# Kernel optimization log

Measured on AMD Instinct MI355X. Metric: run time of the kernel, lower is better.

## Reference

```python
import jax, jax.numpy as jnp
import numpy as np

N_AGENTS = 10000
N_TARGETS = 10000
N_EDGES = 320000
IN_CH = 8
DS = 32          # n_channels // 2 per GAT preprocessor
NCH = 64         # n_channels
C = 128          # 2 * n_channels hidden width
OUT = 2
N_TAPS = 3
N_LAYERS = 2
RADIUS = 2.0
K_NBR = 10       # max_num_neighbors in radius_graph
BIG = 1e9


def radius_nbrs(qpos, kpos, radius, k, exclude_self):
    """For each query point, indices of <=k nearest key points within radius."""
    d2 = jnp.sum((qpos[:, None, :] - kpos[None, :, :]) ** 2, axis=-1)  # [Nq, Nk]
    if exclude_self:
        n = qpos.shape[0]
        d2 = d2.at[jnp.arange(n), jnp.arange(n)].set(BIG)
    d2 = jnp.where(d2 <= radius * radius, d2, BIG)
    negv, idx = jax.lax.top_k(-d2, k)   # nearest-k (deterministic stand-in for PyG's first-k)
    valid = negv > -BIG * 0.5           # [Nq, k] True where a real in-radius neighbor
    return idx, valid


def gatv2(src_feats, dst_feats, idx, valid, Wl, Wr, att, b):
    """Single-head GATv2Conv over a fixed-K neighbor list (idx indexes src_feats)."""
    xl = src_feats @ Wl                      # [Ns, H] messages
    xr = dst_feats @ Wr                      # [Nd, H]
    g = jax.nn.leaky_relu(xl[idx] + xr[:, None, :], 0.2)   # [Nd, K, H]
    s = jnp.einsum('nkh,h->nk', g, att)
    s = jnp.where(valid, s, -BIG)
    s = s - jnp.max(s, axis=1, keepdims=True)
    p = jnp.exp(s) * valid                   # masked exp; isolated nodes -> all-zero
    alpha = p / (jnp.sum(p, axis=1, keepdims=True) + 1e-16)
    return jnp.einsum('nk,nkh->nh', alpha, xl[idx]) + b


def graph_filter(x, src, dst, W, b, n):
    """Polynomial graph filter: y = sum_k S^k x W_k + b, S = unweighted adjacency."""
    y = x @ W[0]
    h = x
    for k in range(1, W.shape[0]):
        h = jax.ops.segment_sum(h[src], dst, num_segments=n)  # one shift tap
        y = y + h @ W[k]
    return y + b


def setup_inputs() -> dict:
    key = jax.random.key(0)
    ks = jax.random.split(key, 16)
    f32 = jnp.float32
    return {
        'own_obs': jax.random.normal(ks[0], (N_AGENTS, IN_CH), dtype=f32),
        'agent_positions': jax.random.uniform(ks[1], (N_AGENTS, 2), dtype=f32) * 100.0,
        'target_positions': jax.random.uniform(ks[2], (N_TARGETS, 2), dtype=f32) * 100.0,
        'W_self': jax.random.normal(ks[3], (IN_CH, NCH), dtype=f32) * 0.1,
        'b_self': jnp.zeros((NCH,), f32),
        'ag_Wl': jax.random.normal(ks[4], (2, DS), dtype=f32) * 0.1,
        'ag_Wr': jax.random.normal(ks[5], (2, DS), dtype=f32) * 0.1,
        'ag_att': jax.random.normal(ks[6], (DS,), dtype=f32) * 0.1,
        'ag_b': jnp.zeros((DS,), f32),
        'tg_Wl': jax.random.normal(ks[7], (2, DS), dtype=f32) * 0.1,
        'tg_Wr': jax.random.normal(ks[8], (2, DS), dtype=f32) * 0.1,
        'tg_att': jax.random.normal(ks[9], (DS,), dtype=f32) * 0.1,
        'tg_b': jnp.zeros((DS,), f32),
        'gf_W': jax.random.normal(ks[10], (N_LAYERS, N_TAPS + 1, C, C), dtype=f32) * (1.0 / np.sqrt(C)),
        'gf_b': jnp.zeros((N_LAYERS, C), f32),
        'bn_gamma': jnp.ones((N_LAYERS, C), f32),
        'bn_beta': jnp.zeros((N_LAYERS, C), f32),
        'W_read': jax.random.normal(ks[11], (C, OUT), dtype=f32) * 0.1,
        'b_read': jnp.zeros((OUT,), f32),
        'edge_index': jax.random.randint(ks[12], (2, N_EDGES), 0, N_AGENTS, dtype=jnp.int32),
    }


def reference(own_obs, agent_positions, target_positions, W_self, b_self,
              ag_Wl, ag_Wr, ag_att, ag_b, tg_Wl, tg_Wr, tg_att, tg_b,
              gf_W, gf_b, bn_gamma, bn_beta, W_read, b_read, edge_index):
    n = agent_positions.shape[0]
    # dynamic radius graphs (agent-agent; target->agent)
    a_idx, a_valid = radius_nbrs(agent_positions, agent_positions, RADIUS, K_NBR, True)
    t_idx, t_valid = radius_nbrs(agent_positions, target_positions, RADIUS, K_NBR, False)

    s = own_obs @ W_self + b_self                                            # self MLP (1 layer)
    a = gatv2(agent_positions, agent_positions, a_idx, a_valid, ag_Wl, ag_Wr, ag_att, ag_b)
    t = gatv2(target_positions, agent_positions, t_idx, t_valid, tg_Wl, tg_Wr, tg_att, tg_b)
    x = jnp.concatenate([s, a, t], axis=1)                                   # [N, 128]

    src, dst = edge_index[0], edge_index[1]
    for l in range(N_LAYERS):
        h = graph_filter(x, src, dst, gf_W[l], gf_b[l], n)
        mu = jnp.mean(h, axis=0)
        var = jnp.var(h, axis=0)
        h = (h - mu) / jnp.sqrt(var + 1e-5) * bn_gamma[l] + bn_beta[l]       # BatchNorm
        x = x + jax.nn.leaky_relu(h, 0.01)                                   # residual block
    return x @ W_read + b_read
```

## Files before the change

### kernel.cpp

```cpp
#include <hip/hip_runtime.h>

typedef unsigned long long u64;
typedef unsigned int u32;
typedef unsigned short ushort_t;

#define NA 10000
#define NE 320000
#define KN 10
#define GRID 50
#define NCELL (GRID * GRID)
#define GATB 157

typedef __attribute__((ext_vector_type(8))) short short8v;
typedef __attribute__((ext_vector_type(4))) float f32x4;

__device__ __forceinline__ u32 f2bf(float f) {
  union { float f; u32 u; } v; v.f = f;
  return (v.u + 0x7fffu + ((v.u >> 16) & 1u)) >> 16;
}
__device__ __forceinline__ float bf2f(u32 b) {
  union { u32 u; float f; } v; v.u = b << 16;
  return v.f;
}

__device__ __forceinline__ void insert10(u64* top, u64 key) {
#pragma unroll
  for (int t = 9; t > 0; --t) {
    u64 prev = top[t - 1];
    u64 cur = top[t];
    top[t] = (key < prev) ? prev : ((key < cur) ? key : cur);
  }
  top[0] = (key < top[0]) ? key : top[0];
}

__device__ __forceinline__ int cell_of(float2 p) {
  int cx = (int)(p.x * 0.5f);
  int cy = (int)(p.y * 0.5f);
  cx = min(max(cx, 0), GRID - 1);
  cy = min(max(cy, 0), GRID - 1);
  return cy * GRID + cx;
}

__global__ __launch_bounds__(256) void k_zero_packw(int* __restrict__ deg, int* __restrict__ cur,
                                                    int* __restrict__ chist, int* __restrict__ ccur,
                                                    const float* __restrict__ gfW,
                                                    ushort_t* __restrict__ Wh, ushort_t* __restrict__ Wlo) {
  int i = blockIdx.x * 256 + threadIdx.x;
  if (i < NA) deg[i] = 0;
  else if (i < 2 * NA) cur[i - NA] = 0;
  else if (i < 2 * NA + 2 * NCELL) chist[i - 2 * NA] = 0;
  else if (i < 2 * NA + 4 * NCELL) ccur[i - 2 * NA - 2 * NCELL] = 0;
  if (i < 131072) {
    int l = i >> 16;
    int rem = i & 65535;
    int t = rem >> 14;
    int k = (rem >> 7) & 127;
    int n = rem & 127;
    float v = gfW[(size_t)i];
    int kt = k >> 5;
    int hi = (k >> 3) & 3;
    int j = k & 7;
    int ct = n >> 4;
    int lane = hi * 16 + (n & 15);
    size_t dst = (((((size_t)(l * 4 + t) * 4 + kt) * 8 + ct) * 64 + lane) * 8 + j);
    u32 h = f2bf(v);
    float r = v - bf2f(h);
    Wh[dst] = (ushort_t)h;
    Wlo[dst] = (ushort_t)f2bf(r);
  }
}

__global__ __launch_bounds__(256) void k_hist_self(const int* __restrict__ edst,
                                                   const float2* __restrict__ apos,
                                                   const float2* __restrict__ tpos,
                                                   int* __restrict__ deg, int* __restrict__ chist,
                                                   const float* __restrict__ own_obs,
                                                   const float* __restrict__ W_self, const float* __restrict__ b_self,
                                                   float* __restrict__ x) {
  __shared__ float sW[512], sb[64];
  int t = threadIdx.x;
  for (int i = t; i < 512; i += 256) sW[i] = W_self[i];
  if (t < 64) sb[t] = b_self[t];
  __syncthreads();
  int i = blockIdx.x * 256 + t;
  if (i < NE) {
    atomicAdd(&deg[edst[i]], 1);
  } else if (i < NE + 2 * NA) {
    int ii = i - NE;
    int graph = (ii >= NA) ? 1 : 0;
    int idx = ii - graph * NA;
    float2 p = graph ? tpos[idx] : apos[idx];
    atomicAdd(&chist[graph * NCELL + cell_of(p)], 1);
  } else if (i < NE + 2 * NA + 8 * NA) {
    int gid = i - NE - 2 * NA;
    int q = gid >> 3;
    int c8 = (gid & 7) * 8;
    const float4* op = (const float4*)(own_obs + (size_t)q * 8);
    float4 o0 = op[0], o1 = op[1];
    float obs[8] = {o0.x, o0.y, o0.z, o0.w, o1.x, o1.y, o1.z, o1.w};
    float out[8];
#pragma unroll
    for (int jj = 0; jj < 8; ++jj) {
      int c = c8 + jj;
      float s = sb[c];
#pragma unroll
      for (int k = 0; k < 8; ++k) s += obs[k] * sW[k * 64 + c];
      out[jj] = s;
    }
    float* xrow = x + (size_t)q * 128 + c8;
    *(float4*)(xrow) = make_float4(out[0], out[1], out[2], out[3]);
    *(float4*)(xrow + 4) = make_float4(out[4], out[5], out[6], out[7]);
  }
}

__global__ __launch_bounds__(1024) void k_scan_all(const int* __restrict__ deg, int* __restrict__ rp,
                                                   const int* __restrict__ chist, int* __restrict__ crp) {
  __shared__ int part[1024];
  int t = threadIdx.x;
  const int* in;
  int* out;
  int per, tot;
  if (blockIdx.x == 0) { in = deg; out = rp; per = 10; tot = NA; }
  else { in = chist; out = crp; per = 5; tot = 2 * NCELL; }
  int beg = min(t * per, tot), end = min(beg + per, tot);
  int s = 0;
  for (int i = beg; i < end; ++i) s += in[i];
  part[t] = s;
  __syncthreads();
  for (int o = 1; o < 1024; o <<= 1) {
    int v = part[t];
    int u = (t >= o) ? part[t - o] : 0;
    __syncthreads();
    part[t] = v + u;
    __syncthreads();
  }
  int base = (t > 0) ? part[t - 1] : 0;
  for (int i = beg; i < end; ++i) { out[i] = base; base += in[i]; }
  if (t == 1023) out[tot] = part[1023];
}

__global__ __launch_bounds__(256) void k_scatter_all(const int* __restrict__ esrc, const int* __restrict__ edst,
                                                     const int* __restrict__ rp, int* __restrict__ cur,
                                                     int* __restrict__ col,
                                                     const float2* __restrict__ apos, const float2* __restrict__ tpos,
                                                     const int* __restrict__ crp, int* __restrict__ ccur,
                                                     float2* __restrict__ ps, int* __restrict__ pid) {
  int i = blockIdx.x * 256 + threadIdx.x;
  if (i < NE) {
    int d = edst[i];
    int p = atomicAdd(&cur[d], 1);
    col[rp[d] + p] = esrc[i];
  } else if (i < NE + 2 * NA) {
    int ii = i - NE;
    int graph = (ii >= NA) ? 1 : 0;
    int idx = ii - graph * NA;
    float2 p = graph ? tpos[idx] : apos[idx];
    int gc = graph * NCELL + cell_of(p);
    int o = crp[gc] + atomicAdd(&ccur[gc], 1);
    ps[o] = p;
    pid[o] = idx;
  }
}

__global__ __launch_bounds__(256) void k_nbr2(const float2* __restrict__ apos,
                                              const int* __restrict__ rp,
                                              const float2* __restrict__ ps, const int* __restrict__ pid,
                                              int* __restrict__ a_idx, int* __restrict__ a_cnt,
                                              int* __restrict__ t_idx, int* __restrict__ t_cnt) {
  int tid = blockIdx.x * 256 + threadIdx.x;
  if (tid >= 2 * NA) return;
  int graph = (tid >= NA) ? 1 : 0;
  int q = tid - graph * NA;
  float2 qp = apos[q];
  int cx = min(max((int)(qp.x * 0.5f), 0), GRID - 1);
  int cy = min(max((int)(qp.y * 0.5f), 0), GRID - 1);

  u64 top[10];
#pragma unroll
  for (int t = 0; t < 10; ++t) top[t] = ~0ull;

  int x0 = max(cx - 1, 0), x1 = min(cx + 1, GRID - 1);
  int y0 = max(cy - 1, 0), y1 = min(cy + 1, GRID - 1);
  for (int yy = y0; yy <= y1; ++yy) {
    int cb = graph * NCELL + yy * GRID + x0;
    int ce = graph * NCELL + yy * GRID + x1;
    int b = rp[cb], e = rp[ce + 1];
    for (int j = b; j < e; ++j) {
      float2 kp = ps[j];
      float dx = qp.x - kp.x;
      float dy = qp.y - kp.y;
      float d2 = __fadd_rn(__fmul_rn(dx, dx), __fmul_rn(dy, dy));
      int g = pid[j];
      if (d2 <= 4.0f && !(graph == 0 && g == q)) {
        u64 key = ((u64)__float_as_uint(d2) << 32) | (u32)g;
        if (key < top[9]) insert10(top, key);
      }
    }
  }
  int cnt = 0;
#pragma unroll
  for (int t = 0; t < 10; ++t) cnt += (top[t] != ~0ull) ? 1 : 0;
  int* oi = graph ? t_idx : a_idx;
#pragma unroll
  for (int t = 0; t < 10; ++t) oi[(size_t)q * 10 + t] = (int)(u32)(top[t] & 0xffffffffu);
  if (graph) t_cnt[q] = cnt; else a_cnt[q] = cnt;
}

__global__ __launch_bounds__(64) void k_gat2(const float2* __restrict__ apos, const float2* __restrict__ tpos,
                                             const int* __restrict__ a_idx, const int* __restrict__ a_cnt,
                                             const int* __restrict__ t_idx, const int* __restrict__ t_cnt,
                                             const float* __restrict__ agWl, const float* __restrict__ agWr,
                                             const float* __restrict__ agatt, const float* __restrict__ agb,
                                             const float* __restrict__ tgWl, const float* __restrict__ tgWr,
                                             const float* __restrict__ tgatt, const float* __restrict__ tgb,
                                             float* __restrict__ x) {
  int graph = (blockIdx.x >= GATB) ? 1 : 0;
  int b0 = blockIdx.x - graph * GATB;
  const float2* srcpos = graph ? tpos : apos;
  const int* idx_all = graph ? t_idx : a_idx;
  const int* cnt_all = graph ? t_cnt : a_cnt;
  const float* Wl = graph ? tgWl : agWl;
  const float* Wr = graph ? tgWr : agWr;
  const float* att = graph ? tgatt : agatt;
  const float* bbp = graph ? tgb : agb;
  int outoff = graph ? 96 : 64;

  __shared__ float sWl[64], sWr[64], satt[32], sbb[32];
  int t = threadIdx.x;
  sWl[t] = Wl[t];
  sWr[t] = Wr[t];
  if (t < 32) { satt[t] = att[t]; sbb[t] = bbp[t]; }
  __syncthreads();
  int q = b0 * 64 + t;
  if (q >= NA) return;
  float2 qp = apos[q];
  float xr[32];
#pragma unroll
  for (int c = 0; c < 32; ++c) xr[c] = qp.x * sWr[c] + qp.y * sWr[32 + c];
  const int* il = idx_all + (size_t)q * 10;
  int cnt = cnt_all[q];
  int idx[10];
#pragma unroll
  for (int k = 0; k < 10; ++k) idx[k] = (k < cnt) ? il[k] : 0;
  float pv[10];
  float m = -1e30f;
#pragma unroll
  for (int k = 0; k < 10; ++k) {
    float2 p = srcpos[idx[k]];
    float s = 0.f;
#pragma unroll
    for (int c = 0; c < 32; ++c) {
      float xl = p.x * sWl[c] + p.y * sWl[32 + c];
      float g = xl + xr[c];
      g = (g >= 0.f) ? g : 0.2f * g;
      s += satt[c] * g;
    }
    pv[k] = s;
    m = (k < cnt) ? fmaxf(m, s) : m;
  }
  float sum = 0.f;
#pragma unroll
  for (int k = 0; k < 10; ++k) {
    float e = (k < cnt) ? expf(pv[k] - m) : 0.f;
    pv[k] = e;
    sum += e;
  }
  float inv = 1.f / (sum + 1e-16f);
  float out[32];
#pragma unroll
  for (int c = 0; c < 32; ++c) out[c] = sbb[c];
#pragma unroll
  for (int k = 0; k < 10; ++k) {
    float a = pv[k] * inv;
    float2 p = srcpos[idx[k]];
#pragma unroll
    for (int c = 0; c < 32; ++c) {
      float xl = p.x * sWl[c] + p.y * sWl[32 + c];
      out[c] += a * xl;
    }
  }
  float* xrow = x + (size_t)q * 128 + outoff;
#pragma unroll
  for (int c4 = 0; c4 < 8; ++c4)
    *(float4*)(xrow + c4 * 4) = make_float4(out[c4 * 4], out[c4 * 4 + 1], out[c4 * 4 + 2], out[c4 * 4 + 3]);
}

__global__ __launch_bounds__(256) void k_shift3(const float* __restrict__ xin, float* __restrict__ xout,
                                                const int* __restrict__ rp, const int* __restrict__ col) {
  int bid = blockIdx.x;
  int half = (bid & 7) >> 2;
  int slot = (bid >> 3) * 4 + (bid & 3);
  if (slot >= 625) return;
  int wid = threadIdx.x >> 6;
  int lane = threadIdx.x & 63;
  int q = lane >> 4;
  int li = lane & 15;
  int row = slot * 16 + wid * 4 + q;
  int beg = rp[row], end = rp[row + 1];
  const f32x4* x4 = (const f32x4*)xin;
  int base = half * 16 + li;
  f32x4 acc = {0.f, 0.f, 0.f, 0.f};
  int j = beg;
  for (; j + 1 < end; j += 2) {
    int s0 = col[j], s1 = col[j + 1];
    f32x4 v0 = x4[(size_t)s0 * 32 + base];
    f32x4 v1 = x4[(size_t)s1 * 32 + base];
    acc += v0;
    acc += v1;
  }
  if (j < end) acc += x4[(size_t)col[j] * 32 + base];
  ((f32x4*)xout)[(size_t)row * 32 + base] = acc;
}

__global__ __launch_bounds__(256) void k_gemm_mfma3(const float* __restrict__ a0, const float* __restrict__ a1,
                                                    const float* __restrict__ a2, const float* __restrict__ a3,
                                                    const ushort_t* __restrict__ Wh, const ushort_t* __restrict__ Wlo,
                                                    const float* __restrict__ b, float* __restrict__ y) {
  const int lane = threadIdx.x & 63;
  const int wave = threadIdx.x >> 6;
  const int ct0 = wave * 2;
  const int row = lane & 15;
  const int hi = lane >> 4;
  const int rb = blockIdx.x * 16;

  f32x4 acc[2];
#pragma unroll
  for (int c = 0; c < 2; ++c) {
    float bv = b[(ct0 + c) * 16 + row];
    acc[c][0] = bv; acc[c][1] = bv; acc[c][2] = bv; acc[c][3] = bv;
  }

  const float* aps[4] = {a0, a1, a2, a3};
#pragma unroll
  for (int t = 0; t < 4; ++t) {
    const float* at = aps[t];
#pragma unroll
    for (int kt = 0; kt < 4; ++kt) {
      const float* ap = at + (size_t)(rb + row) * 128 + kt * 32 + hi * 8;
      float4 fa = *(const float4*)(ap);
      float4 fb = *(const float4*)(ap + 4);
      float av[8] = {fa.x, fa.y, fa.z, fa.w, fb.x, fb.y, fb.z, fb.w};
      short8v ah, al;
#pragma unroll
      for (int j = 0; j < 8; ++j) {
        u32 h = f2bf(av[j]);
        float r = av[j] - bf2f(h);
        ah[j] = (short)h;
        al[j] = (short)f2bf(r);
      }
#pragma unroll
      for (int c = 0; c < 2; ++c) {
        size_t widx = ((((size_t)t * 4 + kt) * 8 + (ct0 + c)) * 64 + lane) * 8;
        short8v bh = *(const short8v*)(Wh + widx);
        short8v bl = *(const short8v*)(Wlo + widx);
        acc[c] = __builtin_amdgcn_mfma_f32_16x16x32_bf16(ah, bh, acc[c], 0, 0, 0);
        acc[c] = __builtin_amdgcn_mfma_f32_16x16x32_bf16(al, bh, acc[c], 0, 0, 0);
        acc[c] = __builtin_amdgcn_mfma_f32_16x16x32_bf16(ah, bl, acc[c], 0, 0, 0);
      }
    }
  }

#pragma unroll
  for (int c = 0; c < 2; ++c) {
#pragma unroll
    for (int r = 0; r < 4; ++r) {
      int grow = rb + hi * 4 + r;
      y[(size_t)grow * 128 + (ct0 + c) * 16 + row] = acc[c][r];
    }
  }
}

__global__ __launch_bounds__(256) void k_bnred(const float* __restrict__ y, double* __restrict__ parts) {
  int c = threadIdx.x & 127;
  int slice = blockIdx.x * 2 + (threadIdx.x >> 7);
  double s = 0.0, ss = 0.0;
  for (int r = slice; r < NA; r += 256) {
    double v = (double)y[(size_t)r * 128 + c];
    s += v;
    ss += v * v;
  }
  parts[(size_t)blockIdx.x * 512 + threadIdx.x] = s;
  parts[(size_t)blockIdx.x * 512 + 256 + threadIdx.x] = ss;
}

__global__ __launch_bounds__(256) void k_bnapply_f(const float* __restrict__ y, const double* __restrict__ parts,
                                                   const float* __restrict__ gamma, const float* __restrict__ beta,
                                                   float* __restrict__ x) {
  __shared__ float sAB[256];
  int t = threadIdx.x;
  if (t < 128) {
    double s = 0.0, ss = 0.0;
    for (int b = 0; b < 128; ++b) {
      const double* p = parts + (size_t)b * 512;
      s += p[t] + p[t + 128];
      ss += p[256 + t] + p[256 + t + 128];
    }
    double mu = s / (double)NA;
    double var = ss / (double)NA - mu * mu;
    double rs = 1.0 / sqrt(var + 1e-5);
    sAB[t] = (float)rs * gamma[t];
    sAB[128 + t] = beta[t] - (float)(mu * rs) * gamma[t];
  }
  __syncthreads();
  const int n4 = NA * 32;
  for (int i = blockIdx.x * 256 + t; i < n4; i += gridDim.x * 256) {
    float4 yv = ((const float4*)y)[i];
    int c = (i & 31) * 4;
    float v0 = yv.x * sAB[c + 0] + sAB[128 + c + 0];
    float v1 = yv.y * sAB[c + 1] + sAB[128 + c + 1];
    float v2 = yv.z * sAB[c + 2] + sAB[128 + c + 2];
    float v3 = yv.w * sAB[c + 3] + sAB[128 + c + 3];
    v0 = (v0 >= 0.f) ? v0 : 0.01f * v0;
    v1 = (v1 >= 0.f) ? v1 : 0.01f * v1;
    v2 = (v2 >= 0.f) ? v2 : 0.01f * v2;
    v3 = (v3 >= 0.f) ? v3 : 0.01f * v3;
    float4 xv = ((float4*)x)[i];
    xv.x += v0; xv.y += v1; xv.z += v2; xv.w += v3;
    ((float4*)x)[i] = xv;
  }
}

__global__ __launch_bounds__(256) void k_read(const float* __restrict__ x, const float* __restrict__ Wr,
                                              const float* __restrict__ br, float* __restrict__ out) {
  int q = blockIdx.x * 256 + threadIdx.x;
  if (q >= NA) return;
  float a0 = br[0], a1 = br[1];
  const float* xr = x + (size_t)q * 128;
#pragma unroll 8
  for (int c = 0; c < 128; ++c) {
    float v = xr[c];
    a0 += v * Wr[c * 2 + 0];
    a1 += v * Wr[c * 2 + 1];
  }
  out[q * 2 + 0] = a0;
  out[q * 2 + 1] = a1;
}

extern "C" void kernel_launch(void* const* d_in, const int* in_sizes, int n_in,
                              void* d_out, int out_size, void* d_ws, size_t ws_size,
                              hipStream_t stream) {
  (void)in_sizes; (void)n_in; (void)out_size; (void)ws_size;
  const float* own_obs = (const float*)d_in[0];
  const float2* apos = (const float2*)d_in[1];
  const float2* tpos = (const float2*)d_in[2];
  const float* W_self = (const float*)d_in[3];
  const float* b_self = (const float*)d_in[4];
  const float* agWl = (const float*)d_in[5];
  const float* agWr = (const float*)d_in[6];
  const float* agatt = (const float*)d_in[7];
  const float* agb = (const float*)d_in[8];
  const float* tgWl = (const float*)d_in[9];
  const float* tgWr = (const float*)d_in[10];
  const float* tgatt = (const float*)d_in[11];
  const float* tgb = (const float*)d_in[12];
  const float* gfW = (const float*)d_in[13];
  const float* gfb = (const float*)d_in[14];
  const float* bng = (const float*)d_in[15];
  const float* bnb = (const float*)d_in[16];
  const float* Wread = (const float*)d_in[17];
  const float* bread = (const float*)d_in[18];
  const int* ei = (const int*)d_in[19];
  const int* esrc = ei;
  const int* edst = ei + NE;

  char* w = (char*)d_ws;
  size_t off = 0;
  auto take = [&](size_t bytes) -> void* {
    void* p = w + off;
    off += (bytes + 255) & ~(size_t)255;
    return p;
  };
  int* a_idx = (int*)take((size_t)NA * KN * 4);
  int* t_idx = (int*)take((size_t)NA * KN * 4);
  int* a_cnt = (int*)take((size_t)NA * 4);
  int* t_cnt = (int*)take((size_t)NA * 4);
  float* x = (float*)take((size_t)NA * 128 * 4);
  float* y = (float*)take((size_t)NA * 128 * 4);
  float* sh1 = (float*)take((size_t)NA * 128 * 4);
  float* sh2 = (float*)take((size_t)NA * 128 * 4);
  float* sh3 = (float*)take((size_t)NA * 128 * 4);
  ushort_t* Wh = (ushort_t*)take((size_t)131072 * 2);
  ushort_t* Wlo = (ushort_t*)take((size_t)131072 * 2);
  double* parts = (double*)take((size_t)128 * 512 * 8);
  int* deg = (int*)take((size_t)NA * 4);
  int* cur = (int*)take((size_t)NA * 4);
  int* rp = (int*)take((size_t)(NA + 1) * 4);
  int* col = (int*)take((size_t)NE * 4);
  int* chist = (int*)take((size_t)2 * NCELL * 4);
  int* crp = (int*)take((size_t)(2 * NCELL + 1) * 4);
  int* ccur = (int*)take((size_t)2 * NCELL * 4);
  float2* ps = (float2*)take((size_t)2 * NA * 8);
  int* pid = (int*)take((size_t)2 * NA * 4);

  k_zero_packw<<<131072 / 256, 256, 0, stream>>>(deg, cur, chist, ccur, gfW, Wh, Wlo);
  k_hist_self<<<(NE + 2 * NA + 8 * NA + 255) / 256, 256, 0, stream>>>(edst, apos, tpos, deg, chist,
                                                                      own_obs, W_self, b_self, x);
  k_scan_all<<<2, 1024, 0, stream>>>(deg, rp, chist, crp);
  k_scatter_all<<<(NE + 2 * NA + 255) / 256, 256, 0, stream>>>(esrc, edst, rp, cur, col,
                                                               apos, tpos, crp, ccur, ps, pid);
  k_nbr2<<<(2 * NA + 255) / 256, 256, 0, stream>>>(apos, crp, ps, pid, a_idx, a_cnt, t_idx, t_cnt);
  k_gat2<<<2 * GATB, 64, 0, stream>>>(apos, tpos, a_idx, a_cnt, t_idx, t_cnt,
                                      agWl, agWr, agatt, agb, tgWl, tgWr, tgatt, tgb, x);

  for (int l = 0; l < 2; ++l) {
    const ushort_t* Whl = Wh + (size_t)l * 65536;
    const ushort_t* Wll = Wlo + (size_t)l * 65536;
    const float* bl = gfb + (size_t)l * 128;
    const float* gl = bng + (size_t)l * 128;
    const float* bb = bnb + (size_t)l * 128;
    k_shift3<<<1256, 256, 0, stream>>>(x, sh1, rp, col);
    k_shift3<<<1256, 256, 0, stream>>>(sh1, sh2, rp, col);
    k_shift3<<<1256, 256, 0, stream>>>(sh2, sh3, rp, col);
    k_gemm_mfma3<<<NA / 16, 256, 0, stream>>>(x, sh1, sh2, sh3, Whl, Wll, bl, y);
    k_bnred<<<128, 256, 0, stream>>>(y, parts);
    k_bnapply_f<<<256, 256, 0, stream>>>(y, parts, gl, bb, x);
  }

  k_read<<<(NA + 255) / 256, 256, 0, stream>>>(x, Wread, bread, (float*)d_out);
}
```

Baseline: 289.6 us.

## Fuse BatchNorm statistics into GEMM epilogue and readout into BN apply

The GEMM now computes per-block per-channel sum and sum-of-squares in double from its accumulators and writes partials, replacing the separate k_bnred pass over y. A single-block k_bnfin kernel reduces the 625 partials into scale/shift, and the final BN-apply kernel also computes the 128->2 readout through wave shuffles, removing k_read. The shift kernel output is written with nontemporal stores. This removes a full read of y per layer and an extra read of x, but adds a serial single-block reduction over 625 partials.

```diff
diff --git a/kernel.cpp b/kernel.cpp
--- a/kernel.cpp
+++ b/kernel.cpp
@@ -309,13 +309,14 @@
     acc += v1;
   }
   if (j < end) acc += x4[(size_t)col[j] * 32 + base];
-  ((f32x4*)xout)[(size_t)row * 32 + base] = acc;
+  __builtin_nontemporal_store(acc, &((f32x4*)xout)[(size_t)row * 32 + base]);
 }
 
 __global__ __launch_bounds__(256) void k_gemm_mfma3(const float* __restrict__ a0, const float* __restrict__ a1,
                                                     const float* __restrict__ a2, const float* __restrict__ a3,
                                                     const ushort_t* __restrict__ Wh, const ushort_t* __restrict__ Wlo,
-                                                    const float* __restrict__ b, float* __restrict__ y) {
+                                                    const float* __restrict__ b, float* __restrict__ y,
+                                                    double* __restrict__ parts) {
   const int lane = threadIdx.x & 63;
   const int wave = threadIdx.x >> 6;
   const int ct0 = wave * 2;
@@ -368,39 +369,53 @@
       y[(size_t)grow * 128 + (ct0 + c) * 16 + row] = acc[c][r];
     }
   }
-}
-
-__global__ __launch_bounds__(256) void k_bnred(const float* __restrict__ y, double* __restrict__ parts) {
-  int c = threadIdx.x & 127;
-  int slice = blockIdx.x * 2 + (threadIdx.x >> 7);
-  double s = 0.0, ss = 0.0;
-  for (int r = slice; r < NA; r += 256) {
-    double v = (double)y[(size_t)r * 128 + c];
-    s += v;
-    ss += v * v;
-  }
-  parts[(size_t)blockIdx.x * 512 + threadIdx.x] = s;
-  parts[(size_t)blockIdx.x * 512 + 256 + threadIdx.x] = ss;
-}
-
-__global__ __launch_bounds__(256) void k_bnapply_f(const float* __restrict__ y, const double* __restrict__ parts,
-                                                   const float* __restrict__ gamma, const float* __restrict__ beta,
-                                                   float* __restrict__ x) {
-  __shared__ float sAB[256];
+
+#pragma unroll
+  for (int c = 0; c < 2; ++c) {
+    double s = 0.0, ss = 0.0;
+#pragma unroll
+    for (int r = 0; r < 4; ++r) {
+      double v = (double)acc[c][r];
+      s += v;
+      ss += v * v;
+    }
+    s += __shfl_xor(s, 16);
+    ss += __shfl_xor(ss, 16);
+    s += __shfl_xor(s, 32);
+    ss += __shfl_xor(ss, 32);
+    if (hi == 0) {
+      int ch = (ct0 + c) * 16 + row;
+      parts[(size_t)blockIdx.x * 256 + ch] = s;
+      parts[(size_t)blockIdx.x * 256 + 128 + ch] = ss;
+    }
+  }
+}
+
+__global__ __launch_bounds__(256) void k_bnfin(const double* __restrict__ parts,
+                                               const float* __restrict__ gamma, const float* __restrict__ beta,
+                                               float* __restrict__ AB) {
+  __shared__ double st[256];
   int t = threadIdx.x;
+  double s = 0.0;
+  for (int b = 0; b < 625; ++b) s += parts[(size_t)b * 256 + t];
+  st[t] = s;
+  __syncthreads();
   if (t < 128) {
-    double s = 0.0, ss = 0.0;
-    for (int b = 0; b < 128; ++b) {
-      const double* p = parts + (size_t)b * 512;
-      s += p[t] + p[t + 128];
-      ss += p[256 + t] + p[256 + t + 128];
-    }
-    double mu = s / (double)NA;
-    double var = ss / (double)NA - mu * mu;
+    double mu = st[t] / (double)NA;
+    double var = st[128 + t] / (double)NA - mu * mu;
     double rs = 1.0 / sqrt(var + 1e-5);
-    sAB[t] = (float)rs * gamma[t];
-    sAB[128 + t] = beta[t] - (float)(mu * rs) * gamma[t];
-  }
+    AB[t] = (float)rs * gamma[t];
+    AB[128 + t] = beta[t] - (float)(mu * rs) * gamma[t];
+  }
+}
+
+__global__ __launch_bounds__(256) void k_bnapply(const float* __restrict__ y, const float* __restrict__ AB,
+                                                 const float* __restrict__ Wread, const float* __restrict__ bread,
+                                                 float* __restrict__ x, float* __restrict__ out, int doread) {
+  __shared__ float sAB[256], sWr[256];
+  int t = threadIdx.x;
+  sAB[t] = AB[t];
+  sWr[t] = Wread[t];
   __syncthreads();
   const int n4 = NA * 32;
   for (int i = blockIdx.x * 256 + t; i < n4; i += gridDim.x * 256) {
@@ -417,23 +432,21 @@
     float4 xv = ((float4*)x)[i];
     xv.x += v0; xv.y += v1; xv.z += v2; xv.w += v3;
     ((float4*)x)[i] = xv;
-  }
-}
-
-__global__ __launch_bounds__(256) void k_read(const float* __restrict__ x, const float* __restrict__ Wr,
-                                              const float* __restrict__ br, float* __restrict__ out) {
-  int q = blockIdx.x * 256 + threadIdx.x;
-  if (q >= NA) return;
-  float a0 = br[0], a1 = br[1];
-  const float* xr = x + (size_t)q * 128;
-#pragma unroll 8
-  for (int c = 0; c < 128; ++c) {
-    float v = xr[c];
-    a0 += v * Wr[c * 2 + 0];
-    a1 += v * Wr[c * 2 + 1];
-  }
-  out[q * 2 + 0] = a0;
-  out[q * 2 + 1] = a1;
+    if (doread) {
+      float a0 = xv.x * sWr[(c + 0) * 2] + xv.y * sWr[(c + 1) * 2] + xv.z * sWr[(c + 2) * 2] + xv.w * sWr[(c + 3) * 2];
+      float a1 = xv.x * sWr[(c + 0) * 2 + 1] + xv.y * sWr[(c + 1) * 2 + 1] + xv.z * sWr[(c + 2) * 2 + 1] + xv.w * sWr[(c + 3) * 2 + 1];
+#pragma unroll
+      for (int o = 1; o < 32; o <<= 1) {
+        a0 += __shfl_xor(a0, o);
+        a1 += __shfl_xor(a1, o);
+      }
+      if ((i & 31) == 0) {
+        int row = i >> 5;
+        out[row * 2 + 0] = a0 + bread[0];
+        out[row * 2 + 1] = a1 + bread[1];
+      }
+    }
+  }
 }
 
 extern "C" void kernel_launch(void* const* d_in, const int* in_sizes, int n_in,
@@ -481,7 +494,8 @@
   float* sh3 = (float*)take((size_t)NA * 128 * 4);
   ushort_t* Wh = (ushort_t*)take((size_t)131072 * 2);
   ushort_t* Wlo = (ushort_t*)take((size_t)131072 * 2);
-  double* parts = (double*)take((size_t)128 * 512 * 8);
+  double* parts = (double*)take((size_t)625 * 256 * 8);
+  float* AB = (float*)take(256 * 4);
   int* deg = (int*)take((size_t)NA * 4);
   int* cur = (int*)take((size_t)NA * 4);
   int* rp = (int*)take((size_t)(NA + 1) * 4);
@@ -511,10 +525,8 @@
     k_shift3<<<1256, 256, 0, stream>>>(x, sh1, rp, col);
     k_shift3<<<1256, 256, 0, stream>>>(sh1, sh2, rp, col);
     k_shift3<<<1256, 256, 0, stream>>>(sh2, sh3, rp, col);
-    k_gemm_mfma3<<<NA / 16, 256, 0, stream>>>(x, sh1, sh2, sh3, Whl, Wll, bl, y);
-    k_bnred<<<128, 256, 0, stream>>>(y, parts);
-    k_bnapply_f<<<256, 256, 0, stream>>>(y, parts, gl, bb, x);
-  }
-
-  k_read<<<(NA + 255) / 256, 256, 0, stream>>>(x, Wread, bread, (float*)d_out);
-}
+    k_gemm_mfma3<<<NA / 16, 256, 0, stream>>>(x, sh1, sh2, sh3, Whl, Wll, bl, y, parts);
+    k_bnfin<<<1, 256, 0, stream>>>(parts, gl, bb, AB);
+    k_bnapply<<<256, 256, 0, stream>>>(y, AB, Wread, bread, x, (float*)d_out, l == 1 ? 1 : 0);
+  }
+}
```

After: 325.2 us. 1.12x slower.
